# Kernel tuning notes

Measured on AMD Instinct MI355X. Metric: run time of the kernel, lower is better.

Reference implementation:

```python
import jax, jax.numpy as jnp
import numpy as np

IN, H1, H2, H3, H4, OUT = 512, 2048, 2048, 1024, 512, 1


def setup_inputs() -> dict:
    key = jax.random.key(0)
    ks = jax.random.split(key, 12)
    def lin(k, fan_in, fan_out):
        # torch Linear default init: U(-1/sqrt(fan_in), 1/sqrt(fan_in))
        bound = 1.0 / np.sqrt(fan_in)
        k1, k2 = jax.random.split(k)
        W = jax.random.uniform(k1, (fan_out, fan_in), jnp.float32, -bound, bound)
        b = jax.random.uniform(k2, (fan_out,), jnp.float32, -bound, bound)
        return W, b
    x = jax.random.normal(ks[0], (16384, IN), jnp.float32)
    cross_w = jnp.ones((IN,), jnp.float32)   # init.constant_(1.0)
    cross_b = jnp.zeros((IN,), jnp.float32)  # init.constant_(0.0)
    W1, b1 = lin(ks[1], IN, H1)
    W2, b2 = lin(ks[2], H1, H2)
    W3, b3 = lin(ks[3], H2, H3)
    W4, b4 = lin(ks[4], H3, H4)
    Wo, bo = lin(ks[5], H4, OUT)
    return {"x": x, "cross_w": cross_w, "cross_b": cross_b,
            "W1": W1, "b1": b1, "W2": W2, "b2": b2,
            "W3": W3, "b3": b3, "W4": W4, "b4": b4,
            "Wo": Wo, "bo": bo}


def reference(x, cross_w, cross_b, W1, b1, W2, b2, W3, b3, W4, b4, Wo, bo):
    # Cross layer: bmm(x0[...,None], x[...,None,:]) . w == x0 * (x . w)
    # (mathematically identical, avoids the O(f^2) outer product)
    xw = x @ cross_w                         # [B]
    h = x * xw[:, None] + cross_b + x        # [B, IN]
    h = jax.nn.relu(h @ W1.T + b1)           # [B, H1]
    h = jax.nn.relu(h @ W2.T + b2)           # [B, H2]
    h = jax.nn.relu(h @ W3.T + b3)           # [B, H3]
    h = jax.nn.relu(h @ W4.T + b4)           # [B, H4]
    return h @ Wo.T + bo                     # [B, OUT]
```

## Files before the change

### kernel.cpp

```cpp
#include <hip/hip_runtime.h>


#define BK 64

typedef __bf16 bf16x8 __attribute__((ext_vector_type(8)));
typedef float  f32x4  __attribute__((ext_vector_type(4)));
typedef unsigned short u16x4 __attribute__((ext_vector_type(4)));

__device__ __forceinline__ unsigned short f2bf(float f) {
    unsigned int u = __builtin_bit_cast(unsigned int, f);
    u += 0x7fffu + ((u >> 16) & 1u);
    return (unsigned short)(u >> 16);
}

__device__ __forceinline__ void async16(const void* g, void* l) {
    __builtin_amdgcn_global_load_lds(
        (const __attribute__((address_space(1))) unsigned int*)g,
        (__attribute__((address_space(3))) unsigned int*)l,
        16, 0, 0);
}

#define BAR()   __builtin_amdgcn_s_barrier()
#define LGKM0() asm volatile("s_waitcnt lgkmcnt(0)" ::: "memory")
#define VMW(n)  asm volatile("s_waitcnt vmcnt(" #n ")" ::: "memory")

#define RDA(RBYTE) do { _Pragma("unroll") \
    for (int f = 0; f < 4; ++f) { \
        af[f][0] = *(const bf16x8*)(aB0 + (RBYTE) + f * 2048); \
        af[f][1] = *(const bf16x8*)(aB1 + (RBYTE) + f * 2048); } } while (0)

#define RDB(DST, RBYTE) do { _Pragma("unroll") \
    for (int c = 0; c < 2; ++c) { \
        DST[c][0] = *(const bf16x8*)(bB0 + (RBYTE) + c * 2048); \
        DST[c][1] = *(const bf16x8*)(bB1 + (RBYTE) + c * 2048); } } while (0)

#define MM16(HA, HB, AF, BF) do { \
    __builtin_amdgcn_s_setprio(1); \
    _Pragma("unroll") for (int f = 0; f < 4; ++f) \
    _Pragma("unroll") for (int c = 0; c < 2; ++c) { \
        acc[HA][f][HB][c] = __builtin_amdgcn_mfma_f32_16x16x32_bf16( \
            AF[f][0], BF[c][0], acc[HA][f][HB][c], 0, 0, 0); \
        acc[HA][f][HB][c] = __builtin_amdgcn_mfma_f32_16x16x32_bf16( \
            AF[f][1], BF[c][1], acc[HA][f][HB][c], 0, 0, 0); } \
    __builtin_amdgcn_s_setprio(0); } while (0)

__global__ __launch_bounds__(512, 1)
void gemm8_bt_bias_relu(const unsigned short* __restrict__ A,
                        const unsigned short* __restrict__ B,
                        const float* __restrict__ bias,
                        unsigned short* __restrict__ C,
                        int M, int N, int K)
{
    __shared__ __align__(16) unsigned short L[65536];
    unsigned short* lds = L;

    constexpr int RA00 = 0,     RA01 = 8192,  RA10 = 16384, RA11 = 24576;
    constexpr int RB00 = 32768, RB01 = 40960, RB10 = 49152, RB11 = 57344;
    constexpr int A00b = 0, A01b = 16384, A10b = 32768, A11b = 49152;
    constexpr int B00b = 0, B01b = 16384, B10b = 32768, B11b = 49152;

    const int tid  = threadIdx.x;
    const int lane = tid & 63;
    const int wave = tid >> 6;
    const int quad = lane >> 4;
    const int l16  = lane & 15;
    const int wr   = wave >> 2;
    const int wc   = wave & 3;

    const int bm = blockIdx.x * 256;
    const int bn = blockIdx.y * 256;

    const int lrow = tid >> 3;
    const int cswz = ((tid & 7) ^ (lrow & 7)) * 8;
    const int tid8 = tid * 8;
    const size_t rstep64 = (size_t)64 * K;
    const unsigned short* gaL = A + (size_t)(bm + lrow) * K + cswz;
    const unsigned short* gaH = gaL + (size_t)128 * K;
    const unsigned short* gbL = B + (size_t)(bn + lrow) * K + cswz;
    const unsigned short* gbH = gbL + (size_t)128 * K;

    auto stage = [&](const unsigned short* g, int region, int ko) {
        async16(g + ko,           lds + region + tid8);
        async16(g + rstep64 + ko, lds + region + 4096 + tid8);
    };

    const int xa = l16 & 7;
    const int c0 = (quad ^ xa) * 8;
    const int c1 = ((quad ^ 4) ^ xa) * 8;
    const int aRd = (64 * wr + l16) * BK;
    const int bRd = (32 * wc + l16) * BK;
    const char* aB0 = (const char*)L + 2 * (aRd + c0);
    const char* aB1 = (const char*)L + 2 * (aRd + c1);
    const char* bB0 = (const char*)L + 65536 + 2 * (bRd + c0);
    const char* bB1 = (const char*)L + 65536 + 2 * (bRd + c1);

    f32x4 acc[2][4][2][2] = {};
    bf16x8 af[4][2], bfl[2][2], bfh[2][2];

    stage(gaL, RA00, 0);
    stage(gbL, RB00, 0);
    stage(gbH, RB01, 0);
    stage(gaH, RA01, 0);
    stage(gaL, RA10, 64);
    stage(gbL, RB10, 64);
    stage(gbH, RB11, 64);
    VMW(6);
    BAR();

    const int nIter = K >> 7;
    for (int i = 0; i < nIter; ++i) {
        const int k1 = (2 * i + 1) << 6;
        int k2 = (2 * i + 2) << 6; if (k2 >= K) k2 -= K;
        int k3 = (2 * i + 3) << 6; if (k3 >= K) k3 -= K;

        RDA(A00b); RDB(bfl, B00b); RDB(bfh, B01b);
        MM16(0, 0, af, bfl);
        stage(gaH, RA11, k1);
        LGKM0();
        BAR();

        MM16(0, 1, af, bfh);
        RDA(A01b);
        stage(gaL, RA00, k2);
        MM16(1, 1, af, bfh);
        stage(gbL, RB00, k2);
        MM16(1, 0, af, bfl);
        stage(gbH, RB01, k2);
        VMW(6);
        BAR();

        RDA(A10b); RDB(bfl, B10b); RDB(bfh, B11b);
        MM16(0, 0, af, bfl);
        stage(gaH, RA01, k2);
        LGKM0();
        BAR();

        MM16(0, 1, af, bfh);
        RDA(A11b);
        stage(gaL, RA10, k3);
        MM16(1, 1, af, bfh);
        stage(gbL, RB10, k3);
        MM16(1, 0, af, bfl);
        stage(gbH, RB11, k3);
        VMW(6);
        BAR();
    }
    VMW(0);

    float bv[2][2];
#pragma unroll
    for (int hb = 0; hb < 2; ++hb)
#pragma unroll
        for (int c = 0; c < 2; ++c)
            bv[hb][c] = bias[bn + hb * 128 + wc * 32 + c * 16 + l16];

#pragma unroll
    for (int ha = 0; ha < 2; ++ha)
#pragma unroll
    for (int f = 0; f < 4; ++f) {
        const int row0 = bm + ha * 128 + wr * 64 + f * 16 + quad * 4;
#pragma unroll
        for (int hb = 0; hb < 2; ++hb)
#pragma unroll
        for (int c = 0; c < 2; ++c) {
            const int col = bn + hb * 128 + wc * 32 + c * 16 + l16;
#pragma unroll
            for (int r = 0; r < 4; ++r) {
                float v = fmaxf(acc[ha][f][hb][c][r] + bv[hb][c], 0.0f);
                C[(size_t)(row0 + r) * N + col] = f2bf(v);
            }
        }
    }
}

__global__ __launch_bounds__(256, 2)
void gemm_bt_head(const unsigned short* __restrict__ A,
                  const unsigned short* __restrict__ B,
                  const float* __restrict__ bias,
                  const float* __restrict__ Wo,
                  float* __restrict__ out,
                  int M, int N, int K)
{
    constexpr int BN = 128;
    constexpr int JT = 4;
    __shared__ __align__(16) unsigned short As[128 * BK];
    __shared__ __align__(16) unsigned short Bs[BN * BK];

    const int tid  = threadIdx.x;
    const int lane = tid & 63;
    const int wave = tid >> 6;
    const int quad = lane >> 4;
    const int l16  = lane & 15;

    const int bm = blockIdx.x * 128;
    const int bn = blockIdx.y * BN;
    const int wm = (wave & 1) * 64;
    const int wn = (wave >> 1) * 64;

    const int lrow = tid >> 3;
    const int gcol = ((tid & 7) ^ (lrow & 7)) * 8;

    const unsigned short* gaBase = A + (size_t)(bm + lrow) * K + gcol;
    const unsigned short* gbBase = B + (size_t)(bn + lrow) * K + gcol;

    unsigned short* lA = As + tid * 8;
    unsigned short* lB = Bs + tid * 8;

    const int xa = l16 & 7;
    const unsigned short* As_w = As + (wm + l16) * BK;
    const unsigned short* Bs_w = Bs + (wn + l16) * BK;
    const int c0 = (quad ^ xa) * 8;
    const int c1 = ((quad ^ 4) ^ xa) * 8;

    f32x4 acc[4][JT] = {};

    for (int k0 = 0; k0 < K; k0 += BK) {
#pragma unroll
        for (int i = 0; i < 4; ++i)
            async16(gaBase + (size_t)(i * 32) * K + k0, lA + i * 2048);
#pragma unroll
        for (int i = 0; i < JT; ++i)
            async16(gbBase + (size_t)(i * 32) * K + k0, lB + i * 2048);
        __syncthreads();

#pragma unroll
        for (int kk = 0; kk < 2; ++kk) {
            const int cs = kk ? c1 : c0;
            bf16x8 af[4], bfr[JT];
#pragma unroll
            for (int i = 0; i < 4; ++i)  af[i]  = *(const bf16x8*)(As_w + i * 16 * BK + cs);
#pragma unroll
            for (int j = 0; j < JT; ++j) bfr[j] = *(const bf16x8*)(Bs_w + j * 16 * BK + cs);
#pragma unroll
            for (int i = 0; i < 4; ++i)
#pragma unroll
                for (int j = 0; j < JT; ++j)
                    acc[i][j] = __builtin_amdgcn_mfma_f32_16x16x32_bf16(
                        af[i], bfr[j], acc[i][j], 0, 0, 0);
        }
        __syncthreads();
    }

    float bv[JT], wov[JT];
#pragma unroll
    for (int j = 0; j < JT; ++j) {
        const int col = bn + wn + j * 16 + l16;
        bv[j]  = bias[col];
        wov[j] = Wo[col];
    }

#pragma unroll
    for (int i = 0; i < 4; ++i) {
#pragma unroll
        for (int r = 0; r < 4; ++r) {
            float ws = 0.f;
#pragma unroll
            for (int j = 0; j < JT; ++j) {
                float v = acc[i][j][r] + bv[j];
                v = fmaxf(v, 0.0f);
                ws += v * wov[j];
            }
#pragma unroll
            for (int off = 8; off > 0; off >>= 1)
                ws += __shfl_xor(ws, off, 64);
            if (l16 == 0) {
                const int row = bm + wm + i * 16 + quad * 4 + r;
                atomicAdd(&out[row], ws);
            }
        }
    }
}

__global__ __launch_bounds__(256)
void prep_kernel(const float* __restrict__ x, const float* __restrict__ cw,
                 const float* __restrict__ cb, unsigned short* __restrict__ h0,
                 const float* __restrict__ s1, const float* __restrict__ s2,
                 const float* __restrict__ s3, const float* __restrict__ s4,
                 unsigned short* __restrict__ d1, unsigned short* __restrict__ d2,
                 unsigned short* __restrict__ d3, unsigned short* __restrict__ d4,
                 const float* __restrict__ bo, float* __restrict__ out)
{
    const int b = blockIdx.x;
    if (b < 7680) {
        long t = (long)b * 256 + threadIdx.x;
        const float* s; unsigned short* d; long off;
        if (t < 262144L)       { s = s1; d = d1; off = t; }
        else if (t < 1310720L) { s = s2; d = d2; off = t - 262144L; }
        else if (t < 1835008L) { s = s3; d = d3; off = t - 1310720L; }
        else                   { s = s4; d = d4; off = t - 1835008L; }
        f32x4 f = *(const f32x4*)(s + off * 4);
        u16x4 o;
#pragma unroll
        for (int i = 0; i < 4; ++i) o[i] = f2bf(f[i]);
        *(u16x4*)(d + off * 4) = o;
    } else if (b < 11776) {
        const int row  = (b - 7680) * 4 + (threadIdx.x >> 6);
        const int lane = threadIdx.x & 63;
        const float* xr = x + (size_t)row * 512;
        float xv[8];
        float s = 0.f;
#pragma unroll
        for (int i = 0; i < 8; ++i) {
            const int c = lane + i * 64;
            xv[i] = xr[c];
            s += xv[i] * cw[c];
        }
#pragma unroll
        for (int off = 32; off > 0; off >>= 1) s += __shfl_down(s, off, 64);
        s = __shfl(s, 0, 64);
        unsigned short* hr = h0 + (size_t)row * 512;
#pragma unroll
        for (int i = 0; i < 8; ++i) {
            const int c = lane + i * 64;
            hr[c] = f2bf(xv[i] * s + cb[c] + xv[i]);
        }
    } else {
        const int t = (b - 11776) * 256 + threadIdx.x;
        out[t] = bo[0];
    }
}

extern "C" void kernel_launch(void* const* d_in, const int* in_sizes, int n_in,
                              void* d_out, int out_size, void* d_ws, size_t ws_size,
                              hipStream_t stream)
{
    const float* x  = (const float*)d_in[0];
    const float* cw = (const float*)d_in[1];
    const float* cb = (const float*)d_in[2];
    const float* W1 = (const float*)d_in[3];  const float* b1 = (const float*)d_in[4];
    const float* W2 = (const float*)d_in[5];  const float* b2 = (const float*)d_in[6];
    const float* W3 = (const float*)d_in[7];  const float* b3 = (const float*)d_in[8];
    const float* W4 = (const float*)d_in[9];  const float* b4 = (const float*)d_in[10];
    const float* Wo = (const float*)d_in[11]; const float* bo = (const float*)d_in[12];
    float* out = (float*)d_out;

    char* p = (char*)d_ws;
    unsigned short* wb1 = (unsigned short*)p; p += (size_t)2048 * 512  * 2;
    unsigned short* wb2 = (unsigned short*)p; p += (size_t)2048 * 2048 * 2;
    unsigned short* wb3 = (unsigned short*)p; p += (size_t)1024 * 2048 * 2;
    unsigned short* wb4 = (unsigned short*)p; p += (size_t)512  * 1024 * 2;
    unsigned short* actA = (unsigned short*)p; p += (size_t)16384 * 2048 * 2;
    unsigned short* actB = (unsigned short*)p;

    prep_kernel<<<11840, 256, 0, stream>>>(x, cw, cb, actA,
                                           W1, W2, W3, W4, wb1, wb2, wb3, wb4,
                                           bo, out);

    gemm8_bt_bias_relu<<<dim3(64, 8), 512, 0, stream>>>(actA, wb1, b1, actB, 16384, 2048, 512);
    gemm8_bt_bias_relu<<<dim3(64, 8), 512, 0, stream>>>(actB, wb2, b2, actA, 16384, 2048, 2048);
    gemm8_bt_bias_relu<<<dim3(64, 4), 512, 0, stream>>>(actA, wb3, b3, actB, 16384, 1024, 2048);
    gemm_bt_head<<<dim3(128, 4), 256, 0, stream>>>(actB, wb4, b4, Wo, out, 16384, 512, 1024);
}
```

Baseline: 358.7 us.

## Replace 8-wave GEMM with 4-wave kernel using 128x128 per-wave tiles

Swaps the 512-thread 256x256-tile hidden-layer GEMM for a 256-thread version in which each wave computes a 128x128 sub-tile. The accumulator grid grows to 8x8 MFMA tiles per wave, and LDS fragments for the two K-halves are ping-ponged in registers. The aim is more MFMA work per LDS read and fewer barriers' worth of wave coordination. In exchange it uses much higher register pressure, has half as many waves to hide latency, and waits on all outstanding global loads (vmcnt 0) every half-iteration, which can stall the prefetch pipeline.

```diff
diff --git a/kernel.cpp b/kernel.cpp
--- a/kernel.cpp
+++ b/kernel.cpp
@@ -24,149 +24,111 @@
 #define LGKM0() asm volatile("s_waitcnt lgkmcnt(0)" ::: "memory")
 #define VMW(n)  asm volatile("s_waitcnt vmcnt(" #n ")" ::: "memory")
 
-#define RDA(RBYTE) do { _Pragma("unroll") \
-    for (int f = 0; f < 4; ++f) { \
-        af[f][0] = *(const bf16x8*)(aB0 + (RBYTE) + f * 2048); \
-        af[f][1] = *(const bf16x8*)(aB1 + (RBYTE) + f * 2048); } } while (0)
-
-#define RDB(DST, RBYTE) do { _Pragma("unroll") \
-    for (int c = 0; c < 2; ++c) { \
-        DST[c][0] = *(const bf16x8*)(bB0 + (RBYTE) + c * 2048); \
-        DST[c][1] = *(const bf16x8*)(bB1 + (RBYTE) + c * 2048); } } while (0)
-
-#define MM16(HA, HB, AF, BF) do { \
-    __builtin_amdgcn_s_setprio(1); \
-    _Pragma("unroll") for (int f = 0; f < 4; ++f) \
-    _Pragma("unroll") for (int c = 0; c < 2; ++c) { \
-        acc[HA][f][HB][c] = __builtin_amdgcn_mfma_f32_16x16x32_bf16( \
-            AF[f][0], BF[c][0], acc[HA][f][HB][c], 0, 0, 0); \
-        acc[HA][f][HB][c] = __builtin_amdgcn_mfma_f32_16x16x32_bf16( \
-            AF[f][1], BF[c][1], acc[HA][f][HB][c], 0, 0, 0); } \
-    __builtin_amdgcn_s_setprio(0); } while (0)
-
-__global__ __launch_bounds__(512, 1)
-void gemm8_bt_bias_relu(const unsigned short* __restrict__ A,
+#define RDFRAG(AF, BF, ABP, BBP, BUF) do { _Pragma("unroll") \
+    for (int f = 0; f < 8; ++f) AF[f] = *(const bf16x8*)((ABP) + (BUF) + f * 2048); \
+    _Pragma("unroll") \
+    for (int g = 0; g < 8; ++g) BF[g] = *(const bf16x8*)((BBP) + (BUF) + g * 2048); } while (0)
+
+#define MM64(AF, BF) do { _Pragma("unroll") \
+    for (int f = 0; f < 8; ++f) _Pragma("unroll") \
+    for (int g = 0; g < 8; ++g) \
+        acc[f][g] = __builtin_amdgcn_mfma_f32_16x16x32_bf16( \
+            AF[f], BF[g], acc[f][g], 0, 0, 0); } while (0)
+
+__global__ __launch_bounds__(256, 1)
+void gemm_fat_bias_relu(const unsigned short* __restrict__ A,
                         const unsigned short* __restrict__ B,
                         const float* __restrict__ bias,
                         unsigned short* __restrict__ C,
                         int M, int N, int K)
 {
     __shared__ __align__(16) unsigned short L[65536];
-    unsigned short* lds = L;
-
-    constexpr int RA00 = 0,     RA01 = 8192,  RA10 = 16384, RA11 = 24576;
-    constexpr int RB00 = 32768, RB01 = 40960, RB10 = 49152, RB11 = 57344;
-    constexpr int A00b = 0, A01b = 16384, A10b = 32768, A11b = 49152;
-    constexpr int B00b = 0, B01b = 16384, B10b = 32768, B11b = 49152;
 
     const int tid  = threadIdx.x;
     const int lane = tid & 63;
     const int wave = tid >> 6;
     const int quad = lane >> 4;
     const int l16  = lane & 15;
-    const int wr   = wave >> 2;
-    const int wc   = wave & 3;
+    const int wr   = wave >> 1;
+    const int wcol = wave & 1;
 
     const int bm = blockIdx.x * 256;
     const int bn = blockIdx.y * 256;
 
-    const int lrow = tid >> 3;
-    const int cswz = ((tid & 7) ^ (lrow & 7)) * 8;
-    const int tid8 = tid * 8;
-    const size_t rstep64 = (size_t)64 * K;
-    const unsigned short* gaL = A + (size_t)(bm + lrow) * K + cswz;
+    const int trow = tid >> 3;
+    const int cswz = ((tid & 7) ^ (trow & 7)) * 8;
+    const unsigned short* gaL = A + (size_t)(bm + trow) * K + cswz;
     const unsigned short* gaH = gaL + (size_t)128 * K;
-    const unsigned short* gbL = B + (size_t)(bn + lrow) * K + cswz;
+    const unsigned short* gbL = B + (size_t)(bn + trow) * K + cswz;
     const unsigned short* gbH = gbL + (size_t)128 * K;
 
-    auto stage = [&](const unsigned short* g, int region, int ko) {
-        async16(g + ko,           lds + region + tid8);
-        async16(g + rstep64 + ko, lds + region + 4096 + tid8);
+    auto stage4 = [&](const unsigned short* g, int regionByte, int ko) {
+#pragma unroll
+        for (int i = 0; i < 4; ++i)
+            async16(g + (size_t)(i * 32) * K + ko,
+                    (char*)L + regionByte + tid * 16 + i * 4096);
     };
 
     const int xa = l16 & 7;
     const int c0 = (quad ^ xa) * 8;
     const int c1 = ((quad ^ 4) ^ xa) * 8;
-    const int aRd = (64 * wr + l16) * BK;
-    const int bRd = (32 * wc + l16) * BK;
-    const char* aB0 = (const char*)L + 2 * (aRd + c0);
-    const char* aB1 = (const char*)L + 2 * (aRd + c1);
-    const char* bB0 = (const char*)L + 65536 + 2 * (bRd + c0);
-    const char* bB1 = (const char*)L + 65536 + 2 * (bRd + c1);
-
-    f32x4 acc[2][4][2][2] = {};
-    bf16x8 af[4][2], bfl[2][2], bfh[2][2];
-
-    stage(gaL, RA00, 0);
-    stage(gbL, RB00, 0);
-    stage(gbH, RB01, 0);
-    stage(gaH, RA01, 0);
-    stage(gaL, RA10, 64);
-    stage(gbL, RB10, 64);
-    stage(gbH, RB11, 64);
-    VMW(6);
+    const char* aB0 = (const char*)L + wr * 16384 + (l16 * 64 + c0) * 2;
+    const char* aB1 = (const char*)L + wr * 16384 + (l16 * 64 + c1) * 2;
+    const char* bB0 = (const char*)L + 65536 + wcol * 16384 + (l16 * 64 + c0) * 2;
+    const char* bB1 = (const char*)L + 65536 + wcol * 16384 + (l16 * 64 + c1) * 2;
+
+    f32x4 acc[8][8] = {};
+    bf16x8 af0[8], bf0[8], af1[8], bf1[8];
+
+    stage4(gaL, 0, 0);     stage4(gaH, 16384, 0);
+    stage4(gbL, 65536, 0); stage4(gbH, 81920, 0);
+    stage4(gaL, 32768, 64);  stage4(gaH, 49152, 64);
+    stage4(gbL, 98304, 64);  stage4(gbH, 114688, 64);
+    VMW(16);
     BAR();
+    RDFRAG(af0, bf0, aB0, bB0, 0);
 
     const int nIter = K >> 7;
     for (int i = 0; i < nIter; ++i) {
-        const int k1 = (2 * i + 1) << 6;
         int k2 = (2 * i + 2) << 6; if (k2 >= K) k2 -= K;
         int k3 = (2 * i + 3) << 6; if (k3 >= K) k3 -= K;
 
-        RDA(A00b); RDB(bfl, B00b); RDB(bfh, B01b);
-        MM16(0, 0, af, bfl);
-        stage(gaH, RA11, k1);
+        RDFRAG(af1, bf1, aB1, bB1, 0);
+        MM64(af0, bf0);
         LGKM0();
+        VMW(0);
         BAR();
-
-        MM16(0, 1, af, bfh);
-        RDA(A01b);
-        stage(gaL, RA00, k2);
-        MM16(1, 1, af, bfh);
-        stage(gbL, RB00, k2);
-        MM16(1, 0, af, bfl);
-        stage(gbH, RB01, k2);
-        VMW(6);
+        stage4(gaL, 0, k2);     stage4(gaH, 16384, k2);
+        stage4(gbL, 65536, k2); stage4(gbH, 81920, k2);
+        RDFRAG(af0, bf0, aB0, bB0, 32768);
+        MM64(af1, bf1);
+
+        RDFRAG(af1, bf1, aB1, bB1, 32768);
+        MM64(af0, bf0);
+        LGKM0();
+        VMW(0);
         BAR();
-
-        RDA(A10b); RDB(bfl, B10b); RDB(bfh, B11b);
-        MM16(0, 0, af, bfl);
-        stage(gaH, RA01, k2);
-        LGKM0();
-        BAR();
-
-        MM16(0, 1, af, bfh);
-        RDA(A11b);
-        stage(gaL, RA10, k3);
-        MM16(1, 1, af, bfh);
-        stage(gbL, RB10, k3);
-        MM16(1, 0, af, bfl);
-        stage(gbH, RB11, k3);
-        VMW(6);
-        BAR();
+        stage4(gaL, 32768, k3);  stage4(gaH, 49152, k3);
+        stage4(gbL, 98304, k3);  stage4(gbH, 114688, k3);
+        RDFRAG(af0, bf0, aB0, bB0, 0);
+        MM64(af1, bf1);
     }
     VMW(0);
 
-    float bv[2][2];
-#pragma unroll
-    for (int hb = 0; hb < 2; ++hb)
-#pragma unroll
-        for (int c = 0; c < 2; ++c)
-            bv[hb][c] = bias[bn + hb * 128 + wc * 32 + c * 16 + l16];
-
-#pragma unroll
-    for (int ha = 0; ha < 2; ++ha)
-#pragma unroll
-    for (int f = 0; f < 4; ++f) {
-        const int row0 = bm + ha * 128 + wr * 64 + f * 16 + quad * 4;
-#pragma unroll
-        for (int hb = 0; hb < 2; ++hb)
-#pragma unroll
-        for (int c = 0; c < 2; ++c) {
-            const int col = bn + hb * 128 + wc * 32 + c * 16 + l16;
+    float bv[8];
+#pragma unroll
+    for (int g = 0; g < 8; ++g)
+        bv[g] = bias[bn + wcol * 128 + g * 16 + l16];
+
+#pragma unroll
+    for (int f = 0; f < 8; ++f) {
+        const int row0 = bm + wr * 128 + f * 16 + quad * 4;
+#pragma unroll
+        for (int g = 0; g < 8; ++g) {
+            const int col = bn + wcol * 128 + g * 16 + l16;
 #pragma unroll
             for (int r = 0; r < 4; ++r) {
-                float v = fmaxf(acc[ha][f][hb][c][r] + bv[hb][c], 0.0f);
+                float v = fmaxf(acc[f][g][r] + bv[g], 0.0f);
                 C[(size_t)(row0 + r) * N + col] = f2bf(v);
             }
         }
@@ -346,8 +308,8 @@
                                            W1, W2, W3, W4, wb1, wb2, wb3, wb4,
                                            bo, out);
 
-    gemm8_bt_bias_relu<<<dim3(64, 8), 512, 0, stream>>>(actA, wb1, b1, actB, 16384, 2048, 512);
-    gemm8_bt_bias_relu<<<dim3(64, 8), 512, 0, stream>>>(actB, wb2, b2, actA, 16384, 2048, 2048);
-    gemm8_bt_bias_relu<<<dim3(64, 4), 512, 0, stream>>>(actA, wb3, b3, actB, 16384, 1024, 2048);
+    gemm_fat_bias_relu<<<dim3(64, 8), 256, 0, stream>>>(actA, wb1, b1, actB, 16384, 2048, 512);
+    gemm_fat_bias_relu<<<dim3(64, 8), 256, 0, stream>>>(actB, wb2, b2, actA, 16384, 2048, 2048);
+    gemm_fat_bias_relu<<<dim3(64, 4), 256, 0, stream>>>(actA, wb3, b3, actB, 16384, 1024, 2048);
     gemm_bt_head<<<dim3(128, 4), 256, 0, stream>>>(actB, wb4, b4, Wo, out, 16384, 512, 1024);
 }
```

Result: slower. 404.8 us (+12.9%).
